# Optimization experiments

Measured on AMD Instinct MI355X. Metric: run time of the kernel, lower is better.

Reference implementation:

```python
import jax, jax.numpy as jnp
import numpy as np

N_NODES = 14   # input_size: nodes of the graph
SEQ = 24       # seq_len == GAT in/out feature dim == output_size
GAT_HID = 64
MLP_HID = 64
NEG_SLOPE = 0.2  # PyG GATConv default leaky_relu slope
B = 32768
N_EDGES = 56


def setup_inputs() -> dict:
    key = jax.random.key(0)
    ks = jax.random.split(key, 16)
    def w(k, shape, fan_in):
        return jax.random.normal(k, shape, dtype=jnp.float32) / np.sqrt(fan_in)
    return {
        "x": jax.random.normal(ks[0], (B, SEQ, N_NODES), dtype=jnp.float32),
        "edge_index": jax.random.randint(ks[1], (2, N_EDGES), 0, N_NODES, dtype=jnp.int64),
        # GATConv 1: in=24 -> out=64, heads=1
        "W1": w(ks[2], (SEQ, GAT_HID), SEQ),
        "a_src1": w(ks[3], (GAT_HID,), GAT_HID),
        "a_dst1": w(ks[4], (GAT_HID,), GAT_HID),
        "b1": jnp.zeros((GAT_HID,), dtype=jnp.float32),
        # GATConv 2: in=64 -> out=24, heads=1
        "W2": w(ks[5], (GAT_HID, SEQ), GAT_HID),
        "a_src2": w(ks[6], (SEQ,), SEQ),
        "a_dst2": w(ks[7], (SEQ,), SEQ),
        "b2": jnp.zeros((SEQ,), dtype=jnp.float32),
        # per-node 2-layer MLPs (one Linear(24,64)+ReLU+Linear(64,24) per node)
        "fc1_w": w(ks[8], (N_NODES, SEQ, MLP_HID), SEQ),
        "fc1_b": jnp.zeros((N_NODES, MLP_HID), dtype=jnp.float32),
        "fc2_w": w(ks[9], (N_NODES, MLP_HID, SEQ), MLP_HID),
        "fc2_b": jnp.zeros((N_NODES, SEQ), dtype=jnp.float32),
    }


def _gat_conv(x, src, dst, W, a_s, a_d, b):
    # PyG GATConv, heads=1, concat=False: linear -> edge attention -> edge softmax over dst -> scatter-sum
    h = x @ W                                             # [N, F]
    alpha = jax.nn.leaky_relu(h[src] @ a_s + h[dst] @ a_d, NEG_SLOPE)  # [E]
    m = jax.ops.segment_max(alpha, dst, num_segments=N_NODES)
    e = jnp.exp(alpha - m[dst])
    s = jax.ops.segment_sum(e, dst, num_segments=N_NODES)
    w = e / s[dst]
    return jax.ops.segment_sum(h[src] * w[:, None], dst, num_segments=N_NODES) + b


def reference(x, edge_index, W1, a_src1, a_dst1, b1, W2, a_src2, a_dst2, b2,
              fc1_w, fc1_b, fc2_w, fc2_b):
    ei = edge_index.astype(jnp.int32)
    loops = jnp.arange(N_NODES, dtype=jnp.int32)  # add_self_loops=True (PyG default)
    src = jnp.concatenate([ei[0], loops])
    dst = jnp.concatenate([ei[1], loops])

    def gat(xs):  # xs: [N_NODES, SEQ]
        h = jax.nn.elu(_gat_conv(xs, src, dst, W1, a_src1, a_dst1, b1))
        return _gat_conv(h, src, dst, W2, a_src2, a_dst2, b2)

    # x: [B, SEQ, N_NODES] -> transpose(1,2) -> per-sample GAT, vmapped over batch
    g = jax.vmap(gat)(x.transpose(0, 2, 1))              # [B, N_NODES, SEQ]
    # per-node 2-layer MLP, batched over nodes via einsum
    h = jax.nn.relu(jnp.einsum('bnf,nfh->bnh', g, fc1_w) + fc1_b)
    pred = jnp.einsum('bnh,nho->bno', h, fc2_w) + fc2_b  # [B, N_NODES, SEQ]
    return pred.transpose(1, 0, 2)                       # [N_NODES, B, SEQ]
```

## Files before the change

kernel.cpp:

```cpp
#include <hip/hip_runtime.h>

typedef unsigned int uu32;

#define NN 14
#define FD 24
#define HD 64
#define NE 70
#define BB 32768
#define SPW 4
#define WPB 4
#define K1_BLOCKS (BB / (WPB * SPW))
#define K2_BLOCKS (NN * (BB / 256))
#define HAP 68
#define H2P 28

__global__ __launch_bounds__(256) void gat_k(
    const float* __restrict__ x, const int* __restrict__ ei,
    const float* __restrict__ W1, const float* __restrict__ as1,
    const float* __restrict__ ad1, const float* __restrict__ b1,
    const float* __restrict__ W2, const float* __restrict__ as2,
    const float* __restrict__ ad2, const float* __restrict__ b2,
    float* __restrict__ Gout) {
    __shared__ __align__(16) float XS[WPB][NN * FD];
    __shared__ __align__(16) float HA[WPB][NN * HAP];
    __shared__ __align__(16) float H2S[WPB][NN * H2P];
    __shared__ __align__(16) float PS[WPB][256];
    __shared__ float sdS[WPB][2 * NN];
    __shared__ float smS[WPB][NN];
    __shared__ __align__(16) float a1S[2 * HD];
    __shared__ __align__(16) float a2S[2 * FD];
    __shared__ int esS[NE], edS[NE];

    const int tid = threadIdx.x;
    const int wv = tid >> 6;
    const int lane = tid & 63;
    float* XSw = XS[wv];
    float* HAw = HA[wv];
    float* H2w = H2S[wv];
    float* Pw = PS[wv];
    float* sdw = sdS[wv];
    float* smw = smS[wv];

    if (tid < 2 * HD) a1S[tid] = (tid < HD) ? as1[tid] : ad1[tid - HD];
    if (tid < 2 * FD) a2S[tid] = (tid < FD) ? as2[tid] : ad2[tid - FD];
    if (tid < 56) {
        int e64 = 1;
        for (int i = 0; i < 8; i++)
            if (ei[2 * i + 1] != 0 || (uu32)ei[2 * i] >= (uu32)NN) e64 = 0;
        esS[tid] = e64 ? ei[2 * tid] : ei[tid];
        edS[tid] = e64 ? ei[112 + 2 * tid] : ei[56 + tid];
    } else if (tid < NE) {
        esS[tid] = tid - 56;
        edS[tid] = tid - 56;
    }

    float w1r[FD];
#pragma unroll
    for (int f = 0; f < FD; f++) w1r[f] = W1[f * HD + lane];
    const float b1r = b1[lane];
    const int f2 = lane % FD;
    const int g2 = lane / FD;
    float w2r[HD];
#pragma unroll
    for (int k = 0; k < HD; k++) w2r[k] = W2[k * FD + f2];
    const float b2r = b2[f2];
    __syncthreads();
    const bool ex = (lane < NE - 64);
    const int s0 = esS[lane], d0 = edS[lane];
    const int s1 = esS[ex ? 64 + lane : 0], d1 = edS[ex ? 64 + lane : 0];

    const int gw = blockIdx.x * WPB + wv;
    for (int t = 0; t < SPW; t++) {
        const size_t b = (size_t)gw * SPW + t;
        const float4* xb4 = (const float4*)(x + b * (NN * FD));
        {
            float4 v = xb4[lane];
            int e = 4 * lane;
            XSw[(e % NN) * FD + (e / NN)] = v.x; e++;
            XSw[(e % NN) * FD + (e / NN)] = v.y; e++;
            XSw[(e % NN) * FD + (e / NN)] = v.z; e++;
            XSw[(e % NN) * FD + (e / NN)] = v.w;
            if (lane < 20) {
                v = xb4[64 + lane];
                e = 256 + 4 * lane;
                XSw[(e % NN) * FD + (e / NN)] = v.x; e++;
                XSw[(e % NN) * FD + (e / NN)] = v.y; e++;
                XSw[(e % NN) * FD + (e / NN)] = v.z; e++;
                XSw[(e % NN) * FD + (e / NN)] = v.w;
            }
        }
        __syncthreads();
        float acc[NN];
#pragma unroll
        for (int n = 0; n < NN; n++) acc[n] = 0.0f;
#pragma unroll
        for (int k = 0; k < 6; k++) {
#pragma unroll
            for (int n = 0; n < NN; n++) {
                float4 xv = *(const float4*)&XSw[n * FD + 4 * k];
                acc[n] = fmaf(xv.x, w1r[4 * k + 0], acc[n]);
                acc[n] = fmaf(xv.y, w1r[4 * k + 1], acc[n]);
                acc[n] = fmaf(xv.z, w1r[4 * k + 2], acc[n]);
                acc[n] = fmaf(xv.w, w1r[4 * k + 3], acc[n]);
            }
        }
#pragma unroll
        for (int n = 0; n < NN; n++) HAw[n * HAP + lane] = acc[n];
        __syncthreads();
        if (lane < 2 * NN) {
            const int v = (lane >= NN) ? 1 : 0;
            const int n2 = lane - v * NN;
            float s = 0.0f;
#pragma unroll
            for (int k = 0; k < 16; k++) {
                float4 h4 = *(const float4*)&HAw[n2 * HAP + 4 * k];
                float4 a4 = *(const float4*)&a1S[v * HD + 4 * k];
                s = fmaf(h4.x, a4.x, s); s = fmaf(h4.y, a4.y, s);
                s = fmaf(h4.z, a4.z, s); s = fmaf(h4.w, a4.w, s);
            }
            sdw[v * NN + n2] = s;
        }
        *(float4*)&Pw[lane * 4] = make_float4(0.f, 0.f, 0.f, 0.f);
        if (lane < NN) smw[lane] = 0.0f;
        __syncthreads();
        {
            float a = sdw[s0] + sdw[NN + d0];
            a = a > 0.0f ? a : 0.2f * a;
            float e0 = __expf(a);
            atomicAdd(&smw[d0], e0);
            atomicAdd(&Pw[d0 * 16 + s0], e0);
            if (ex) {
                a = sdw[s1] + sdw[NN + d1];
                a = a > 0.0f ? a : 0.2f * a;
                float e1 = __expf(a);
                atomicAdd(&smw[d1], e1);
                atomicAdd(&Pw[d1 * 16 + s1], e1);
            }
        }
        __syncthreads();
        float acc2[NN];
#pragma unroll
        for (int n = 0; n < NN; n++) {
            float a = 0.0f;
#pragma unroll
            for (int k4 = 0; k4 < 3; k4++) {
                float4 p4 = *(const float4*)&Pw[n * 16 + 4 * k4];
                a = fmaf(p4.x, acc[4 * k4 + 0], a);
                a = fmaf(p4.y, acc[4 * k4 + 1], a);
                a = fmaf(p4.z, acc[4 * k4 + 2], a);
                a = fmaf(p4.w, acc[4 * k4 + 3], a);
            }
            float4 p4 = *(const float4*)&Pw[n * 16 + 12];
            a = fmaf(p4.x, acc[12], a);
            a = fmaf(p4.y, acc[13], a);
            a = __fdividef(a, smw[n]) + b1r;
            acc2[n] = a > 0.0f ? a : (__expf(a) - 1.0f);
        }
#pragma unroll
        for (int n = 0; n < NN; n++) HAw[n * HAP + lane] = acc2[n];
        __syncthreads();
        if (g2 < 2) {
#pragma unroll
            for (int i = 0; i < 7; i++) {
                const int n = g2 + 2 * i;
                float a = 0.0f;
#pragma unroll
                for (int k4 = 0; k4 < 16; k4++) {
                    float4 v4 = *(const float4*)&HAw[n * HAP + 4 * k4];
                    a = fmaf(v4.x, w2r[4 * k4 + 0], a);
                    a = fmaf(v4.y, w2r[4 * k4 + 1], a);
                    a = fmaf(v4.z, w2r[4 * k4 + 2], a);
                    a = fmaf(v4.w, w2r[4 * k4 + 3], a);
                }
                H2w[n * H2P + f2] = a;
            }
        }
        __syncthreads();
        if (lane < 2 * NN) {
            const int v = (lane >= NN) ? 1 : 0;
            const int n2 = lane - v * NN;
            float s = 0.0f;
#pragma unroll
            for (int q = 0; q < 6; q++) {
                float4 h4 = *(const float4*)&H2w[n2 * H2P + 4 * q];
                float4 a4 = *(const float4*)&a2S[v * FD + 4 * q];
                s = fmaf(h4.x, a4.x, s); s = fmaf(h4.y, a4.y, s);
                s = fmaf(h4.z, a4.z, s); s = fmaf(h4.w, a4.w, s);
            }
            sdw[v * NN + n2] = s;
        }
        *(float4*)&Pw[lane * 4] = make_float4(0.f, 0.f, 0.f, 0.f);
        if (lane < NN) smw[lane] = 0.0f;
        __syncthreads();
        {
            float a = sdw[s0] + sdw[NN + d0];
            a = a > 0.0f ? a : 0.2f * a;
            float e0 = __expf(a);
            atomicAdd(&smw[d0], e0);
            atomicAdd(&Pw[d0 * 16 + s0], e0);
            if (ex) {
                a = sdw[s1] + sdw[NN + d1];
                a = a > 0.0f ? a : 0.2f * a;
                float e1 = __expf(a);
                atomicAdd(&smw[d1], e1);
                atomicAdd(&Pw[d1 * 16 + s1], e1);
            }
        }
        __syncthreads();
        if (g2 < 2) {
            float h2c[NN];
#pragma unroll
            for (int k = 0; k < NN; k++) h2c[k] = H2w[k * H2P + f2];
#pragma unroll
            for (int i = 0; i < 7; i++) {
                const int n = g2 + 2 * i;
                float a = 0.0f;
#pragma unroll
                for (int k4 = 0; k4 < 3; k4++) {
                    float4 p4 = *(const float4*)&Pw[n * 16 + 4 * k4];
                    a = fmaf(p4.x, h2c[4 * k4 + 0], a);
                    a = fmaf(p4.y, h2c[4 * k4 + 1], a);
                    a = fmaf(p4.z, h2c[4 * k4 + 2], a);
                    a = fmaf(p4.w, h2c[4 * k4 + 3], a);
                }
                float4 p4 = *(const float4*)&Pw[n * 16 + 12];
                a = fmaf(p4.x, h2c[12], a);
                a = fmaf(p4.y, h2c[13], a);
                Gout[((size_t)n * BB + b) * FD + f2] =
                    __fdividef(a, smw[n]) + b2r;
            }
        }
        __syncthreads();
    }
}

__global__ __launch_bounds__(256) void mlp_k(
    const float* __restrict__ fc1w, const float* __restrict__ fc1b,
    const float* __restrict__ fc2w, const float* __restrict__ fc2b,
    float* gio) {
    __shared__ __align__(16) float W1L[FD * HD];
    __shared__ __align__(16) float W2L[HD * FD];
    __shared__ float B1L[HD];
    __shared__ float B2L[FD];

    const int t = threadIdx.x;
    const int n = blockIdx.x >> 7;
    const int b0 = (blockIdx.x & 127) * 256;

    const float4* w1p = (const float4*)(fc1w + (size_t)n * (FD * HD));
    const float4* w2p = (const float4*)(fc2w + (size_t)n * (HD * FD));
    for (int i = t; i < 384; i += 256) {
        *(float4*)&W1L[4 * i] = w1p[i];
        *(float4*)&W2L[4 * i] = w2p[i];
    }
    if (t < HD) B1L[t] = fc1b[n * HD + t];
    if (t < FD) B2L[t] = fc2b[n * FD + t];
    __syncthreads();

    const size_t base = ((size_t)n * BB + b0 + t) * FD;
    float g[FD], o[FD];
#pragma unroll
    for (int q = 0; q < 6; q++)
        *(float4*)&g[4 * q] = *(const float4*)&gio[base + 4 * q];
#pragma unroll
    for (int f = 0; f < FD; f++) o[f] = B2L[f];

#pragma unroll
    for (int j4 = 0; j4 < 16; j4++) {
        float h0 = B1L[4 * j4 + 0], h1 = B1L[4 * j4 + 1];
        float h2 = B1L[4 * j4 + 2], h3 = B1L[4 * j4 + 3];
#pragma unroll
        for (int f = 0; f < FD; f++) {
            float4 w4 = *(const float4*)&W1L[f * HD + 4 * j4];
            h0 = fmaf(g[f], w4.x, h0);
            h1 = fmaf(g[f], w4.y, h1);
            h2 = fmaf(g[f], w4.z, h2);
            h3 = fmaf(g[f], w4.w, h3);
        }
        h0 = fmaxf(h0, 0.f); h1 = fmaxf(h1, 0.f);
        h2 = fmaxf(h2, 0.f); h3 = fmaxf(h3, 0.f);
        float hv[4] = {h0, h1, h2, h3};
#pragma unroll
        for (int u2 = 0; u2 < 4; u2++) {
            const int j = 4 * j4 + u2;
#pragma unroll
            for (int f4 = 0; f4 < 6; f4++) {
                float4 w4 = *(const float4*)&W2L[j * FD + 4 * f4];
                o[4 * f4 + 0] = fmaf(hv[u2], w4.x, o[4 * f4 + 0]);
                o[4 * f4 + 1] = fmaf(hv[u2], w4.y, o[4 * f4 + 1]);
                o[4 * f4 + 2] = fmaf(hv[u2], w4.z, o[4 * f4 + 2]);
                o[4 * f4 + 3] = fmaf(hv[u2], w4.w, o[4 * f4 + 3]);
            }
        }
    }
#pragma unroll
    for (int q = 0; q < 6; q++)
        *(float4*)&gio[base + 4 * q] = *(const float4*)&o[4 * q];
}

extern "C" void kernel_launch(void* const* d_in, const int* in_sizes, int n_in,
                              void* d_out, int out_size, void* d_ws, size_t ws_size,
                              hipStream_t stream) {
    (void)in_sizes; (void)n_in; (void)out_size; (void)d_ws; (void)ws_size;
    const float* x    = (const float*)d_in[0];
    const int*   ei   = (const int*)d_in[1];
    const float* W1   = (const float*)d_in[2];
    const float* as1  = (const float*)d_in[3];
    const float* ad1  = (const float*)d_in[4];
    const float* b1   = (const float*)d_in[5];
    const float* W2   = (const float*)d_in[6];
    const float* as2  = (const float*)d_in[7];
    const float* ad2  = (const float*)d_in[8];
    const float* b2   = (const float*)d_in[9];
    const float* fc1w = (const float*)d_in[10];
    const float* fc1b = (const float*)d_in[11];
    const float* fc2w = (const float*)d_in[12];
    const float* fc2b = (const float*)d_in[13];
    float* gio = (float*)d_out;

    gat_k<<<dim3(K1_BLOCKS), dim3(256), 0, stream>>>(
        x, ei, W1, as1, ad1, b1, W2, as2, ad2, b2, gio);
    mlp_k<<<dim3(K2_BLOCKS), dim3(256), 0, stream>>>(
        fc1w, fc1b, fc2w, fc2b, gio);
}
```

Before: 343.0 us.

## Replace block barriers with wave-local LDS waits and read MLP weights from global

In the GAT kernel each wave works on its own slice of shared memory, so the block-wide barriers are replaced with a wave-level LDS wait (s_waitcnt lgkmcnt(0)), and the per-wave P buffer is shrunk to 224 floats. The MLP kernel drops its shared-memory staging of weights and reads them through uniform global loads (likely scalar/cached), with the outer loop no longer unrolled. This removes barrier stalls and LDS staging, but depends on lockstep execution within a wave for correctness, and global weight reads may cost more latency than LDS.

```diff
diff --git a/kernel.cpp b/kernel.cpp
--- a/kernel.cpp
+++ b/kernel.cpp
@@ -13,6 +13,9 @@
 #define K2_BLOCKS (NN * (BB / 256))
 #define HAP 68
 #define H2P 28
+#define PSZ 224
+
+#define WSYNC() asm volatile("s_waitcnt lgkmcnt(0)" ::: "memory")
 
 __global__ __launch_bounds__(256) void gat_k(
     const float* __restrict__ x, const int* __restrict__ ei,
@@ -24,7 +27,7 @@
     __shared__ __align__(16) float XS[WPB][NN * FD];
     __shared__ __align__(16) float HA[WPB][NN * HAP];
     __shared__ __align__(16) float H2S[WPB][NN * H2P];
-    __shared__ __align__(16) float PS[WPB][256];
+    __shared__ __align__(16) float PS[WPB][PSZ];
     __shared__ float sdS[WPB][2 * NN];
     __shared__ float smS[WPB][NN];
     __shared__ __align__(16) float a1S[2 * HD];
@@ -89,7 +92,7 @@
                 XSw[(e % NN) * FD + (e / NN)] = v.w;
             }
         }
-        __syncthreads();
+        WSYNC();
         float acc[NN];
 #pragma unroll
         for (int n = 0; n < NN; n++) acc[n] = 0.0f;
@@ -106,7 +109,7 @@
         }
 #pragma unroll
         for (int n = 0; n < NN; n++) HAw[n * HAP + lane] = acc[n];
-        __syncthreads();
+        WSYNC();
         if (lane < 2 * NN) {
             const int v = (lane >= NN) ? 1 : 0;
             const int n2 = lane - v * NN;
@@ -120,9 +123,10 @@
             }
             sdw[v * NN + n2] = s;
         }
-        *(float4*)&Pw[lane * 4] = make_float4(0.f, 0.f, 0.f, 0.f);
+        if (lane < PSZ / 4)
+            *(float4*)&Pw[lane * 4] = make_float4(0.f, 0.f, 0.f, 0.f);
         if (lane < NN) smw[lane] = 0.0f;
-        __syncthreads();
+        WSYNC();
         {
             float a = sdw[s0] + sdw[NN + d0];
             a = a > 0.0f ? a : 0.2f * a;
@@ -137,7 +141,7 @@
                 atomicAdd(&Pw[d1 * 16 + s1], e1);
             }
         }
-        __syncthreads();
+        WSYNC();
         float acc2[NN];
 #pragma unroll
         for (int n = 0; n < NN; n++) {
@@ -158,7 +162,7 @@
         }
 #pragma unroll
         for (int n = 0; n < NN; n++) HAw[n * HAP + lane] = acc2[n];
-        __syncthreads();
+        WSYNC();
         if (g2 < 2) {
 #pragma unroll
             for (int i = 0; i < 7; i++) {
@@ -175,7 +179,7 @@
                 H2w[n * H2P + f2] = a;
             }
         }
-        __syncthreads();
+        WSYNC();
         if (lane < 2 * NN) {
             const int v = (lane >= NN) ? 1 : 0;
             const int n2 = lane - v * NN;
@@ -189,9 +193,10 @@
             }
             sdw[v * NN + n2] = s;
         }
-        *(float4*)&Pw[lane * 4] = make_float4(0.f, 0.f, 0.f, 0.f);
+        if (lane < PSZ / 4)
+            *(float4*)&Pw[lane * 4] = make_float4(0.f, 0.f, 0.f, 0.f);
         if (lane < NN) smw[lane] = 0.0f;
-        __syncthreads();
+        WSYNC();
         {
             float a = sdw[s0] + sdw[NN + d0];
             a = a > 0.0f ? a : 0.2f * a;
@@ -206,7 +211,7 @@
                 atomicAdd(&Pw[d1 * 16 + s1], e1);
             }
         }
-        __syncthreads();
+        WSYNC();
         if (g2 < 2) {
             float h2c[NN];
 #pragma unroll
@@ -230,32 +235,22 @@
                     __fdividef(a, smw[n]) + b2r;
             }
         }
-        __syncthreads();
+        WSYNC();
     }
 }
 
 __global__ __launch_bounds__(256) void mlp_k(
     const float* __restrict__ fc1w, const float* __restrict__ fc1b,
     const float* __restrict__ fc2w, const float* __restrict__ fc2b,
-    float* gio) {
-    __shared__ __align__(16) float W1L[FD * HD];
-    __shared__ __align__(16) float W2L[HD * FD];
-    __shared__ float B1L[HD];
-    __shared__ float B2L[FD];
-
+    float* __restrict__ gio) {
     const int t = threadIdx.x;
     const int n = blockIdx.x >> 7;
     const int b0 = (blockIdx.x & 127) * 256;
 
-    const float4* w1p = (const float4*)(fc1w + (size_t)n * (FD * HD));
-    const float4* w2p = (const float4*)(fc2w + (size_t)n * (HD * FD));
-    for (int i = t; i < 384; i += 256) {
-        *(float4*)&W1L[4 * i] = w1p[i];
-        *(float4*)&W2L[4 * i] = w2p[i];
-    }
-    if (t < HD) B1L[t] = fc1b[n * HD + t];
-    if (t < FD) B2L[t] = fc2b[n * FD + t];
-    __syncthreads();
+    const float* __restrict__ W1 = fc1w + (size_t)n * (FD * HD);
+    const float* __restrict__ W2 = fc2w + (size_t)n * (HD * FD);
+    const float* __restrict__ B1 = fc1b + n * HD;
+    const float* __restrict__ B2 = fc2b + n * FD;
 
     const size_t base = ((size_t)n * BB + b0 + t) * FD;
     float g[FD], o[FD];
@@ -263,15 +258,15 @@
     for (int q = 0; q < 6; q++)
         *(float4*)&g[4 * q] = *(const float4*)&gio[base + 4 * q];
 #pragma unroll
-    for (int f = 0; f < FD; f++) o[f] = B2L[f];
-
-#pragma unroll
+    for (int f = 0; f < FD; f++) o[f] = B2[f];
+
+#pragma unroll 1
     for (int j4 = 0; j4 < 16; j4++) {
-        float h0 = B1L[4 * j4 + 0], h1 = B1L[4 * j4 + 1];
-        float h2 = B1L[4 * j4 + 2], h3 = B1L[4 * j4 + 3];
+        float h0 = B1[4 * j4 + 0], h1 = B1[4 * j4 + 1];
+        float h2 = B1[4 * j4 + 2], h3 = B1[4 * j4 + 3];
 #pragma unroll
         for (int f = 0; f < FD; f++) {
-            float4 w4 = *(const float4*)&W1L[f * HD + 4 * j4];
+            float4 w4 = *(const float4*)&W1[f * HD + 4 * j4];
             h0 = fmaf(g[f], w4.x, h0);
             h1 = fmaf(g[f], w4.y, h1);
             h2 = fmaf(g[f], w4.z, h2);
@@ -285,7 +280,7 @@
             const int j = 4 * j4 + u2;
 #pragma unroll
             for (int f4 = 0; f4 < 6; f4++) {
-                float4 w4 = *(const float4*)&W2L[j * FD + 4 * f4];
+                float4 w4 = *(const float4*)&W2[j * FD + 4 * f4];
                 o[4 * f4 + 0] = fmaf(hv[u2], w4.x, o[4 * f4 + 0]);
                 o[4 * f4 + 1] = fmaf(hv[u2], w4.y, o[4 * f4 + 1]);
                 o[4 * f4 + 2] = fmaf(hv[u2], w4.z, o[4 * f4 + 2]);
```

Result: slower. 351.7 us (+2.5%).
